# Kernel tuning notes

Measured on AMD Instinct MI355X. Metric: run time of the kernel, lower is better.

## Reference

```python
import jax, jax.numpy as jnp
import numpy as np

L, N, D, B_, T = 4, 4, 2048, 2, 2048  # num_blocks, expansion_rate, dim, batch, seq


def setup_inputs() -> dict:
    key = jax.random.key(0)
    ks = jax.random.split(key, 12)
    f = lambda k, sh, s=0.02: s * jax.random.normal(k, sh, jnp.float32)
    x = jax.random.normal(ks[0], (B_, T, D), jnp.float32)
    # structural torch inits + small noise so grads/kernels are exercised
    eyecols = jnp.stack([jnp.eye(N, dtype=jnp.float32)[:, [i % N]] for i in range(L)])  # [L,N,1]
    A_m = eyecols + f(ks[1], (L, N, 1), 0.05)
    A_r = jnp.broadcast_to(jnp.eye(N, dtype=jnp.float32), (L, N, N)) + f(ks[2], (L, N, N), 0.05)
    Bp = jnp.ones((L, 1, N), jnp.float32) + f(ks[3], (L, 1, N), 0.05)
    W_m = f(ks[4], (L, D, 1))
    W_r = f(ks[5], (L, D, N))
    W_b = f(ks[6], (L, D, N))
    s_a = 0.01 * jnp.ones((L, 1, 1), jnp.float32)
    s_b = 0.01 * jnp.ones((L, 1, 1), jnp.float32)
    dyn_gamma = jnp.ones((L, D), jnp.float32) + f(ks[7], (L, D), 0.05)   # LayerNorm(bias=False)
    norm_gamma = jnp.ones((L, D), jnp.float32) + f(ks[8], (L, D), 0.05)  # per-block norm weight
    norm_beta = f(ks[9], (L, D))                                          # per-block norm bias
    Wblk = f(ks[10], (L, D, D), 1.0) / np.sqrt(D)                         # block = Linear(D, D)
    bblk = f(ks[11], (L, D))
    return dict(x=x, A_m=A_m, A_r=A_r, Bp=Bp, W_m=W_m, W_r=W_r, W_b=W_b,
                s_a=s_a, s_b=s_b, dyn_gamma=dyn_gamma, norm_gamma=norm_gamma,
                norm_beta=norm_beta, Wblk=Wblk, bblk=bblk)


def _ln(x, gamma, beta=None, eps=1e-5):
    mu = jnp.mean(x, axis=-1, keepdims=True)
    var = jnp.mean(jnp.square(x - mu), axis=-1, keepdims=True)
    y = (x - mu) * jax.lax.rsqrt(var + eps) * gamma
    return y if beta is None else y + beta


def reference(x, A_m, A_r, Bp, W_m, W_r, W_b, s_a, s_b,
              dyn_gamma, norm_gamma, norm_beta, Wblk, bblk):
    # hyper branch (n > 0), dynamic=True, pre_norm=True
    H = jnp.repeat(x[:, :, None, :], N, axis=2)  # [B,T,N,D]
    for i in range(L):
        # ---- width connections ----
        Hn = _ln(H, dyn_gamma[i])                                              # dynamic LN, no bias
        Am = A_m[i] + s_a[i] * jnp.tanh(jnp.einsum('btnd,do->btno', Hn, W_m[i]))  # [B,T,N,1]
        Ar = A_r[i] + s_a[i] * jnp.tanh(jnp.einsum('btnd,dm->btnm', Hn, W_r[i]))  # [B,T,N,N]
        WC = jnp.concatenate([Am, Ar], axis=-1)                                # [B,T,N,1+N]
        Ht = jnp.einsum('btnd,btnm->btdm', H, WC)                              # H^T @ WC
        h = Ht[..., 0]                                                         # [B,T,D]
        H = jnp.swapaxes(Ht[..., 1:], -2, -1)                                  # [B,T,N,D]
        # ---- pre-norm + block ----
        h = _ln(h, norm_gamma[i], norm_beta[i])
        h = jnp.einsum('btd,de->bte', h, Wblk[i]) + bblk[i]
        # ---- depth connections ----
        hn = _ln(h, dyn_gamma[i])
        Bv = Bp[i][0] + s_b[i] * jnp.tanh(jnp.einsum('btd,dn->btn', hn, W_b[i]))  # [B,T,N]
        H = H + h[:, :, None, :] * Bv[..., None]
    return H.sum(axis=2)  # [B,T,D]
```

## Files before the change

kernel.cpp:

```cpp
#include <hip/hip_runtime.h>
#include <hip/hip_bf16.h>


#define DD 2048
#define NN 4
#define LL 4
#define NTOK 4096
#define EPSF 1e-5f

typedef __attribute__((ext_vector_type(8))) short bf16x8;
typedef __attribute__((ext_vector_type(4))) float f32x4;

__device__ __forceinline__ float bf2f(short u) {
  union { unsigned int i; float f; } v;
  v.i = ((unsigned int)(unsigned short)u) << 16;
  return v.f;
}
__device__ __forceinline__ short f2bf(float f) {
  union { float f; unsigned int i; } v; v.f = f;
  unsigned int x = v.i;
  return (short)((x + 0x7fffu + ((x >> 16) & 1u)) >> 16);
}
__device__ __forceinline__ float wred(float v) {
#pragma unroll
  for (int off = 32; off > 0; off >>= 1) v += __shfl_xor(v, off, 64);
  return v;
}
__device__ __forceinline__ void ld16(const void* g, void* l) {
  __builtin_amdgcn_global_load_lds(
      (const __attribute__((address_space(1))) void*)g,
      (__attribute__((address_space(3))) void*)l, 16, 0, 0);
}

__global__ __launch_bounds__(256) void prep_pack(
    const float* __restrict__ W_r, const float* __restrict__ W_b,
    short* __restrict__ wrb, short* __restrict__ wbb) {
  const int i = blockIdx.x * 256 + threadIdx.x;
  f32x4 r = *(const f32x4*)(W_r + (size_t)i * 4);
  f32x4 b = *(const f32x4*)(W_b + (size_t)i * 4);
  short ro[4], bo[4];
#pragma unroll
  for (int k = 0; k < 4; k++) { ro[k] = f2bf(r[k]); bo[k] = f2bf(b[k]); }
  *(unsigned long long*)(wrb + (size_t)i * 4) = *(unsigned long long*)ro;
  *(unsigned long long*)(wbb + (size_t)i * 4) = *(unsigned long long*)bo;
}

__global__ __launch_bounds__(64) void prep_sums(
    const float* __restrict__ W_m, const float* __restrict__ W_r,
    const float* __restrict__ W_b, const float* __restrict__ dyn_gamma,
    float* __restrict__ S0w, float* __restrict__ T0d) {
  const int l = blockIdx.x;
  const int lane = threadIdx.x;
  float s[5] = {0, 0, 0, 0, 0}, t[4] = {0, 0, 0, 0};
  for (int d = lane; d < DD; d += 64) {
    const float g = dyn_gamma[l * DD + d];
    s[0] += g * W_m[l * DD + d];
    f32x4 r = *(const f32x4*)(W_r + ((size_t)l * DD + d) * 4);
    f32x4 b = *(const f32x4*)(W_b + ((size_t)l * DD + d) * 4);
#pragma unroll
    for (int m = 0; m < 4; m++) { s[1 + m] += g * r[m]; t[m] += g * b[m]; }
  }
#pragma unroll
  for (int m = 0; m < 5; m++) s[m] = wred(s[m]);
#pragma unroll
  for (int n = 0; n < 4; n++) t[n] = wred(t[n]);
  if (lane == 0) {
#pragma unroll
    for (int m = 0; m < 5; m++) S0w[l * 5 + m] = s[m];
#pragma unroll
    for (int n = 0; n < 4; n++) T0d[l * 4 + n] = t[n];
  }
}

__global__ __launch_bounds__(256) void transpose_wblk(
    const float* __restrict__ W, short* __restrict__ Wt) {
  __shared__ float tile[64][65];
  const int blk = blockIdx.z;
  const int c0 = blockIdx.x * 64;
  const int r0 = blockIdx.y * 64;
  const float* Ws = W + (size_t)blk * DD * DD;
  short* Wd = Wt + (size_t)blk * DD * DD;
  const int tx = threadIdx.x & 63, ty = threadIdx.x >> 6;
#pragma unroll
  for (int r = 0; r < 16; r++) {
    const int row = ty + r * 4;
    tile[row][tx] = Ws[(size_t)(r0 + row) * DD + c0 + tx];
  }
  __syncthreads();
#pragma unroll
  for (int r = 0; r < 16; r++) {
    const int row = ty + r * 4;
    Wd[(size_t)(c0 + row) * DD + r0 + tx] = f2bf(tile[tx][row]);
  }
}

__global__ __launch_bounds__(256) void width0_kernel(
    const float* __restrict__ x, short* __restrict__ Hst,
    short* __restrict__ hnorm, const float* __restrict__ A_m,
    const float* __restrict__ A_r, const float* __restrict__ W_m,
    const short* __restrict__ wrb, const float* __restrict__ s_a,
    const float* __restrict__ dyn_gamma, const float* __restrict__ norm_gamma,
    const float* __restrict__ norm_beta, const float* __restrict__ S0w) {
  const int wave = threadIdx.x >> 6;
  const int lane = threadIdx.x & 63;
  const int tok = blockIdx.x * 4 + wave;
  const int blk = 0;
  const float* dg = dyn_gamma + blk * DD;
  const float* wm = W_m + blk * DD;
  const short* wr = wrb + (size_t)blk * DD * 4;

  bf16x8 hreg[4];
  const float* xr = x + (size_t)tok * DD;
#pragma unroll
  for (int j = 0; j < 4; j++) {
    const int d0 = lane * 8 + j * 512;
    f32x4 a = *(const f32x4*)(xr + d0);
    f32x4 b = *(const f32x4*)(xr + d0 + 4);
    bf16x8 p;
#pragma unroll
    for (int q = 0; q < 4; q++) { p[q] = f2bf(a[q]); p[4 + q] = f2bf(b[q]); }
    hreg[j] = p;
  }

  float sH = 0, sH2 = 0, S1[5] = {0, 0, 0, 0, 0};
#pragma unroll
  for (int j = 0; j < 4; j++) {
    const int d0 = lane * 8 + j * 512;
    f32x4 g0 = *(const f32x4*)(dg + d0), g1 = *(const f32x4*)(dg + d0 + 4);
    f32x4 m0 = *(const f32x4*)(wm + d0), m1 = *(const f32x4*)(wm + d0 + 4);
    bf16x8 wv[4];
#pragma unroll
    for (int p = 0; p < 4; p++)
      wv[p] = *(const bf16x8*)(wr + (size_t)(d0 + 2 * p) * 4);
#pragma unroll
    for (int q = 0; q < 8; q++) {
      const float g = (q < 4) ? g0[q] : g1[q - 4];
      const float wmv = (q < 4) ? m0[q] : m1[q - 4];
      const float hv = bf2f(hreg[j][q]);
      sH += hv; sH2 += hv * hv;
      const float hg = hv * g;
      S1[0] += hg * wmv;
#pragma unroll
      for (int m = 0; m < 4; m++)
        S1[1 + m] += hg * bf2f(wv[q >> 1][(q & 1) * 4 + m]);
    }
  }
  sH = wred(sH); sH2 = wred(sH2);
#pragma unroll
  for (int m = 0; m < 5; m++) S1[m] = wred(S1[m]);

  const float sa = s_a[blk];
  const float mu0 = sH * (1.f / DD);
  const float inv0 = rsqrtf(sH2 * (1.f / DD) - mu0 * mu0 + EPSF);
  float amSum = 0.f, arCol[NN] = {0, 0, 0, 0};
  {
    const float t0 = tanhf(inv0 * (S1[0] - mu0 * S0w[blk * 5 + 0]));
    float tm[NN];
#pragma unroll
    for (int m = 0; m < NN; m++)
      tm[m] = tanhf(inv0 * (S1[1 + m] - mu0 * S0w[blk * 5 + 1 + m]));
#pragma unroll
    for (int n = 0; n < NN; n++) {
      amSum += A_m[blk * NN + n] + sa * t0;
#pragma unroll
      for (int m = 0; m < NN; m++)
        arCol[m] += A_r[blk * NN * NN + n * NN + m] + sa * tm[m];
    }
  }

  short* Ho = Hst + (size_t)tok * NN * DD;
  float hbuf[4][8];
  float sh = 0.f, sh2 = 0.f;
#pragma unroll
  for (int j = 0; j < 4; j++) {
    const int d0 = lane * 8 + j * 512;
    bf16x8 outp[NN];
#pragma unroll
    for (int q = 0; q < 8; q++) {
      const float hv = bf2f(hreg[j][q]);
      const float a0 = hv * amSum;
      hbuf[j][q] = a0; sh += a0; sh2 += a0 * a0;
#pragma unroll
      for (int m = 0; m < NN; m++) outp[m][q] = f2bf(hv * arCol[m]);
    }
#pragma unroll
    for (int m = 0; m < NN; m++) *(bf16x8*)(Ho + m * DD + d0) = outp[m];
  }
  sh = wred(sh); sh2 = wred(sh2);
  const float mu = sh * (1.f / DD);
  const float inv = rsqrtf(sh2 * (1.f / DD) - mu * mu + EPSF);
  const float* ng = norm_gamma + blk * DD;
  const float* nb = norm_beta + blk * DD;
  short* hn = hnorm + (size_t)tok * DD;
#pragma unroll
  for (int j = 0; j < 4; j++) {
    const int d0 = lane * 8 + j * 512;
    f32x4 g0 = *(const f32x4*)(ng + d0), g1 = *(const f32x4*)(ng + d0 + 4);
    f32x4 b0 = *(const f32x4*)(nb + d0), b1 = *(const f32x4*)(nb + d0 + 4);
    bf16x8 o;
#pragma unroll
    for (int q = 0; q < 8; q++) {
      const float g = (q < 4) ? g0[q] : g1[q - 4];
      const float b = (q < 4) ? b0[q] : b1[q - 4];
      o[q] = f2bf((hbuf[j][q] - mu) * inv * g + b);
    }
    *(bf16x8*)(hn + d0) = o;
  }
}

__global__ __launch_bounds__(256) void gemm_kernel(
    const short* __restrict__ A, const short* __restrict__ Bt,
    const float* __restrict__ bias, short* __restrict__ C) {
  __shared__ short lA[2][128 * 64];
  __shared__ short lB[2][128 * 64];
  const int tid = threadIdx.x;
  const int lane = tid & 63;
  const int wave = tid >> 6;
  const int m0 = blockIdx.x * 128, n0 = blockIdx.y * 128;
  const int wm = wave >> 1, wn = wave & 1;

  f32x4 acc[4][4] = {};

#define STAGE(buf, kt)                                                        \
  {                                                                           \
    const int k0 = (kt) * 64;                                                 \
    _Pragma("unroll") for (int c = 0; c < 4; c++) {                           \
      const int idx = c * 256 + tid;                                          \
      const int row = idx >> 3;                                               \
      const int colsw = (((idx & 7) ^ (row & 7)) * 8);                        \
      ld16(A + (size_t)(m0 + row) * DD + k0 + colsw,                          \
           (char*)&lA[buf][0] + idx * 16);                                    \
      ld16(Bt + (size_t)(n0 + row) * DD + k0 + colsw,                         \
           (char*)&lB[buf][0] + idx * 16);                                    \
    }                                                                         \
  }

  STAGE(0, 0);
  __syncthreads();

  for (int kt = 0; kt < 32; ++kt) {
    const int cur = kt & 1;
    if (kt < 31) STAGE(cur ^ 1, kt + 1);
    const char* bufA = (const char*)&lA[cur][0];
    const char* bufB = (const char*)&lB[cur][0];
#pragma unroll
    for (int kk = 0; kk < 2; ++kk) {
      const int gsw = (kk * 64 + (lane >> 4) * 16) ^ ((lane & 7) << 4);
      bf16x8 af[4], bfr[4];
#pragma unroll
      for (int m = 0; m < 4; m++) {
        const int r = wm * 64 + m * 16 + (lane & 15);
        af[m] = *(const bf16x8*)(bufA + r * 128 + gsw);
      }
#pragma unroll
      for (int n = 0; n < 4; n++) {
        const int r = wn * 64 + n * 16 + (lane & 15);
        bfr[n] = *(const bf16x8*)(bufB + r * 128 + gsw);
      }
#pragma unroll
      for (int m = 0; m < 4; m++)
#pragma unroll
        for (int n = 0; n < 4; n++)
          acc[m][n] = __builtin_amdgcn_mfma_f32_16x16x32_bf16(
              af[m], bfr[n], acc[m][n], 0, 0, 0);
    }
    __syncthreads();
  }
#undef STAGE

#pragma unroll
  for (int n = 0; n < 4; n++) {
    const int col = n0 + wn * 64 + n * 16 + (lane & 15);
    const float bv = bias[col];
#pragma unroll
    for (int m = 0; m < 4; m++) {
      const int rbase = m0 + wm * 64 + m * 16 + ((lane >> 4) << 2);
#pragma unroll
      for (int j = 0; j < 4; j++)
        C[(size_t)(rbase + j) * DD + col] = f2bf(acc[m][n][j] + bv);
    }
  }
}

__global__ __launch_bounds__(256) void fused_dw(
    const short* __restrict__ h2, short* __restrict__ Hst,
    short* __restrict__ hnorm, const float* __restrict__ Bp,
    const short* __restrict__ wbb, const float* __restrict__ s_b,
    const float* __restrict__ A_m, const float* __restrict__ A_r,
    const float* __restrict__ W_m, const short* __restrict__ wrb,
    const float* __restrict__ s_a, const float* __restrict__ dyn_gamma,
    const float* __restrict__ norm_gamma, const float* __restrict__ norm_beta,
    const float* __restrict__ S0w, const float* __restrict__ T0d, int blk) {
  const int wave = threadIdx.x >> 6;
  const int lane = threadIdx.x & 63;
  const int tok = blockIdx.x * 4 + wave;
  const int nblk = blk + 1;
  const short* hr = h2 + (size_t)tok * DD;
  short* Ho = Hst + (size_t)tok * NN * DD;

  bf16x8 h2r[4], hold[NN][4];
#pragma unroll
  for (int j = 0; j < 4; j++) {
    const int d0 = lane * 8 + j * 512;
    h2r[j] = *(const bf16x8*)(hr + d0);
#pragma unroll
    for (int n = 0; n < NN; n++)
      hold[n][j] = *(const bf16x8*)(Ho + n * DD + d0);
  }

  const float* dgd = dyn_gamma + blk * DD;
  const short* wb = wbb + (size_t)blk * DD * 4;
  float s1 = 0.f, s2 = 0.f, T1[NN] = {0, 0, 0, 0};
#pragma unroll
  for (int j = 0; j < 4; j++) {
    const int d0 = lane * 8 + j * 512;
    f32x4 g0 = *(const f32x4*)(dgd + d0), g1 = *(const f32x4*)(dgd + d0 + 4);
    bf16x8 wv[4];
#pragma unroll
    for (int p = 0; p < 4; p++)
      wv[p] = *(const bf16x8*)(wb + (size_t)(d0 + 2 * p) * 4);
#pragma unroll
    for (int q = 0; q < 8; q++) {
      const float g = (q < 4) ? g0[q] : g1[q - 4];
      const float hv = bf2f(h2r[j][q]);
      s1 += hv; s2 += hv * hv;
      const float hg = hv * g;
#pragma unroll
      for (int n = 0; n < NN; n++)
        T1[n] += hg * bf2f(wv[q >> 1][(q & 1) * 4 + n]);
    }
  }
  s1 = wred(s1); s2 = wred(s2);
#pragma unroll
  for (int n = 0; n < NN; n++) T1[n] = wred(T1[n]);
  float Bv[NN];
  {
    const float mu = s1 * (1.f / DD);
    const float inv = rsqrtf(s2 * (1.f / DD) - mu * mu + EPSF);
    const float sb = s_b[blk];
#pragma unroll
    for (int n = 0; n < NN; n++)
      Bv[n] = Bp[blk * NN + n] +
              sb * tanhf(inv * (T1[n] - mu * T0d[blk * NN + n]));
  }
#pragma unroll
  for (int n = 0; n < NN; n++)
#pragma unroll
    for (int j = 0; j < 4; j++) {
      bf16x8 o;
#pragma unroll
      for (int q = 0; q < 8; q++)
        o[q] = f2bf(bf2f(hold[n][j][q]) + bf2f(h2r[j][q]) * Bv[n]);
      hold[n][j] = o;
    }

  const float* dg = dyn_gamma + nblk * DD;
  const float* wm = W_m + nblk * DD;
  const short* wr = wrb + (size_t)nblk * DD * 4;
  float sH[NN] = {0, 0, 0, 0}, sH2[NN] = {0, 0, 0, 0};
  float S1[NN][5];
#pragma unroll
  for (int n = 0; n < NN; n++)
#pragma unroll
    for (int m = 0; m < 5; m++) S1[n][m] = 0.f;

#pragma unroll
  for (int j = 0; j < 4; j++) {
    const int d0 = lane * 8 + j * 512;
    f32x4 g0 = *(const f32x4*)(dg + d0), g1 = *(const f32x4*)(dg + d0 + 4);
    f32x4 m0 = *(const f32x4*)(wm + d0), m1 = *(const f32x4*)(wm + d0 + 4);
    bf16x8 wv[4];
#pragma unroll
    for (int p = 0; p < 4; p++)
      wv[p] = *(const bf16x8*)(wr + (size_t)(d0 + 2 * p) * 4);
#pragma unroll
    for (int q = 0; q < 8; q++) {
      const float g = (q < 4) ? g0[q] : g1[q - 4];
      const float wmv = (q < 4) ? m0[q] : m1[q - 4];
      float gw[5];
      gw[0] = g * wmv;
#pragma unroll
      for (int m = 0; m < 4; m++)
        gw[1 + m] = g * bf2f(wv[q >> 1][(q & 1) * 4 + m]);
#pragma unroll
      for (int n = 0; n < NN; n++) {
        const float hv = bf2f(hold[n][j][q]);
        sH[n] += hv; sH2[n] += hv * hv;
#pragma unroll
        for (int m = 0; m < 5; m++) S1[n][m] += hv * gw[m];
      }
    }
  }
#pragma unroll
  for (int n = 0; n < NN; n++) { sH[n] = wred(sH[n]); sH2[n] = wred(sH2[n]); }
#pragma unroll
  for (int n = 0; n < NN; n++)
#pragma unroll
    for (int m = 0; m < 5; m++) S1[n][m] = wred(S1[n][m]);

  const float sa = s_a[nblk];
  float Am[NN], Ar[NN][NN];
#pragma unroll
  for (int n = 0; n < NN; n++) {
    const float mu = sH[n] * (1.f / DD);
    const float var = sH2[n] * (1.f / DD) - mu * mu;
    const float inv = rsqrtf(var + EPSF);
    Am[n] = A_m[nblk * NN + n] +
            sa * tanhf(inv * (S1[n][0] - mu * S0w[nblk * 5 + 0]));
#pragma unroll
    for (int m = 0; m < NN; m++)
      Ar[n][m] = A_r[nblk * NN * NN + n * NN + m] +
                 sa * tanhf(inv * (S1[n][1 + m] - mu * S0w[nblk * 5 + 1 + m]));
  }

  float hbuf[4][8];
  float sh = 0.f, sh2 = 0.f;
#pragma unroll
  for (int j = 0; j < 4; j++) {
    const int d0 = lane * 8 + j * 512;
    bf16x8 outp[NN];
#pragma unroll
    for (int q = 0; q < 8; q++) {
      float a0 = 0.f, am0 = 0.f, am1 = 0.f, am2 = 0.f, am3 = 0.f;
#pragma unroll
      for (int n = 0; n < NN; n++) {
        const float hv = bf2f(hold[n][j][q]);
        a0 += hv * Am[n];
        am0 += hv * Ar[n][0];
        am1 += hv * Ar[n][1];
        am2 += hv * Ar[n][2];
        am3 += hv * Ar[n][3];
      }
      hbuf[j][q] = a0; sh += a0; sh2 += a0 * a0;
      outp[0][q] = f2bf(am0); outp[1][q] = f2bf(am1);
      outp[2][q] = f2bf(am2); outp[3][q] = f2bf(am3);
    }
#pragma unroll
    for (int m = 0; m < NN; m++) *(bf16x8*)(Ho + m * DD + d0) = outp[m];
  }
  sh = wred(sh); sh2 = wred(sh2);
  const float mu = sh * (1.f / DD);
  const float inv = rsqrtf(sh2 * (1.f / DD) - mu * mu + EPSF);
  const float* ng = norm_gamma + nblk * DD;
  const float* nb = norm_beta + nblk * DD;
  short* hn = hnorm + (size_t)tok * DD;
#pragma unroll
  for (int j = 0; j < 4; j++) {
    const int d0 = lane * 8 + j * 512;
    f32x4 g0 = *(const f32x4*)(ng + d0), g1 = *(const f32x4*)(ng + d0 + 4);
    f32x4 b0 = *(const f32x4*)(nb + d0), b1 = *(const f32x4*)(nb + d0 + 4);
    bf16x8 o;
#pragma unroll
    for (int q = 0; q < 8; q++) {
      const float g = (q < 4) ? g0[q] : g1[q - 4];
      const float b = (q < 4) ? b0[q] : b1[q - 4];
      o[q] = f2bf((hbuf[j][q] - mu) * inv * g + b);
    }
    *(bf16x8*)(hn + d0) = o;
  }
}

__global__ __launch_bounds__(256) void depth_last(
    const short* __restrict__ h2, const short* __restrict__ Hst,
    float* __restrict__ out, const float* __restrict__ Bp,
    const short* __restrict__ wbb, const float* __restrict__ s_b,
    const float* __restrict__ dyn_gamma, const float* __restrict__ T0d,
    int blk) {
  const int wave = threadIdx.x >> 6;
  const int lane = threadIdx.x & 63;
  const int tok = blockIdx.x * 4 + wave;
  const short* hr = h2 + (size_t)tok * DD;
  const float* dg = dyn_gamma + blk * DD;
  const short* wb = wbb + (size_t)blk * DD * 4;

  bf16x8 h2r[4];
  float s1 = 0.f, s2 = 0.f, T1[NN] = {0, 0, 0, 0};
#pragma unroll
  for (int j = 0; j < 4; j++) {
    const int d0 = lane * 8 + j * 512;
    h2r[j] = *(const bf16x8*)(hr + d0);
    f32x4 g0 = *(const f32x4*)(dg + d0), g1 = *(const f32x4*)(dg + d0 + 4);
    bf16x8 wv[4];
#pragma unroll
    for (int p = 0; p < 4; p++)
      wv[p] = *(const bf16x8*)(wb + (size_t)(d0 + 2 * p) * 4);
#pragma unroll
    for (int q = 0; q < 8; q++) {
      const float g = (q < 4) ? g0[q] : g1[q - 4];
      const float hv = bf2f(h2r[j][q]);
      s1 += hv; s2 += hv * hv;
      const float hg = hv * g;
#pragma unroll
      for (int n = 0; n < NN; n++)
        T1[n] += hg * bf2f(wv[q >> 1][(q & 1) * 4 + n]);
    }
  }
  s1 = wred(s1); s2 = wred(s2);
#pragma unroll
  for (int n = 0; n < NN; n++) T1[n] = wred(T1[n]);
  const float mu = s1 * (1.f / DD);
  const float inv = rsqrtf(s2 * (1.f / DD) - mu * mu + EPSF);
  const float sb = s_b[blk];
  float bsum = 0.f;
#pragma unroll
  for (int n = 0; n < NN; n++)
    bsum += Bp[blk * NN + n] + sb * tanhf(inv * (T1[n] - mu * T0d[blk * NN + n]));

  const short* Ho = Hst + (size_t)tok * NN * DD;
  float* orow = out + (size_t)tok * DD;
#pragma unroll
  for (int j = 0; j < 4; j++) {
    const int d0 = lane * 8 + j * 512;
    bf16x8 hrow[NN];
#pragma unroll
    for (int n = 0; n < NN; n++) hrow[n] = *(const bf16x8*)(Ho + n * DD + d0);
    f32x4 o0, o1;
#pragma unroll
    for (int q = 0; q < 8; q++) {
      const float hv = bf2f(h2r[j][q]);
      float s = hv * bsum;
#pragma unroll
      for (int n = 0; n < NN; n++) s += bf2f(hrow[n][q]);
      if (q < 4) o0[q] = s; else o1[q - 4] = s;
    }
    *(f32x4*)(orow + d0) = o0;
    *(f32x4*)(orow + d0 + 4) = o1;
  }
}

extern "C" void kernel_launch(void* const* d_in, const int* in_sizes, int n_in,
                              void* d_out, int out_size, void* d_ws,
                              size_t ws_size, hipStream_t stream) {
  const float* x = (const float*)d_in[0];
  const float* A_m = (const float*)d_in[1];
  const float* A_r = (const float*)d_in[2];
  const float* Bp = (const float*)d_in[3];
  const float* W_m = (const float*)d_in[4];
  const float* W_r = (const float*)d_in[5];
  const float* W_b = (const float*)d_in[6];
  const float* s_a = (const float*)d_in[7];
  const float* s_b = (const float*)d_in[8];
  const float* dyn_gamma = (const float*)d_in[9];
  const float* norm_gamma = (const float*)d_in[10];
  const float* norm_beta = (const float*)d_in[11];
  const float* Wblk = (const float*)d_in[12];
  const float* bblk = (const float*)d_in[13];
  float* out = (float*)d_out;

  char* ws = (char*)d_ws;
  short* Hst = (short*)(ws);
  short* hnorm = (short*)(ws + 67108864);
  short* h2 = (short*)(ws + 83886080);
  short* wrb = (short*)(ws + 100663296);
  short* wbb = (short*)(ws + 100663296 + 65536);
  float* S0w = (float*)(ws + 100663296 + 131072);
  float* T0d = (float*)(ws + 100663296 + 131072 + 128);
  short* Wt = (short*)d_out;

  dim3 tb(256);
  prep_pack<<<32, tb, 0, stream>>>(W_r, W_b, wrb, wbb);
  prep_sums<<<4, dim3(64), 0, stream>>>(W_m, W_r, W_b, dyn_gamma, S0w, T0d);
  transpose_wblk<<<dim3(32, 32, 4), tb, 0, stream>>>(Wblk, Wt);
  width0_kernel<<<1024, tb, 0, stream>>>(x, Hst, hnorm, A_m, A_r, W_m, wrb,
                                         s_a, dyn_gamma, norm_gamma, norm_beta,
                                         S0w);
  for (int i = 0; i < LL; i++) {
    gemm_kernel<<<dim3(32, 16), tb, 0, stream>>>(
        hnorm, Wt + (size_t)i * DD * DD, bblk + i * DD, h2);
    if (i < LL - 1)
      fused_dw<<<1024, tb, 0, stream>>>(h2, Hst, hnorm, Bp, wbb, s_b, A_m, A_r,
                                        W_m, wrb, s_a, dyn_gamma, norm_gamma,
                                        norm_beta, S0w, T0d, i);
    else
      depth_last<<<1024, tb, 0, stream>>>(h2, Hst, out, Bp, wbb, s_b,
                                          dyn_gamma, T0d, i);
  }
}
```

Baseline: 392.0 us.

## Fold pre-norm LayerNorm into GEMM epilogue and gamma into packed weights

Stops materialising the normalised block input. The width kernels now write the raw mixed h plus per-token (inv, mu*inv) stats. norm_gamma is folded into the transposed block weight, and precomputed row sums E0/E1 apply the mean-subtraction and beta/bias correction in the GEMM epilogue. dyn_gamma is also prefolded into the packed bf16 W_m/W_r/W_b, which removes gamma loads and multiplies from the width/depth kernels. This cuts a second pass and per-element LN arithmetic, but adds a row_sums kernel, and the mean cancellation now happens after bf16 rounding, which risks precision loss. It also divides norm_beta by norm_gamma.

```diff
diff --git a/kernel.cpp b/kernel.cpp
--- a/kernel.cpp
+++ b/kernel.cpp
@@ -10,6 +10,7 @@
 
 typedef __attribute__((ext_vector_type(8))) short bf16x8;
 typedef __attribute__((ext_vector_type(4))) float f32x4;
+typedef __attribute__((ext_vector_type(2))) float f32x2;
 
 __device__ __forceinline__ float bf2f(short u) {
   union { unsigned int i; float f; } v;
@@ -17,9 +18,10 @@
   return v.f;
 }
 __device__ __forceinline__ short f2bf(float f) {
-  union { float f; unsigned int i; } v; v.f = f;
-  unsigned int x = v.i;
-  return (short)((x + 0x7fffu + ((x >> 16) & 1u)) >> 16);
+  __hip_bfloat16 h = __float2bfloat16(f);
+  short s;
+  __builtin_memcpy(&s, &h, 2);
+  return s;
 }
 __device__ __forceinline__ float wred(float v) {
 #pragma unroll
@@ -33,16 +35,22 @@
 }
 
 __global__ __launch_bounds__(256) void prep_pack(
-    const float* __restrict__ W_r, const float* __restrict__ W_b,
-    short* __restrict__ wrb, short* __restrict__ wbb) {
+    const float* __restrict__ W_m, const float* __restrict__ W_r,
+    const float* __restrict__ W_b, const float* __restrict__ dyn_gamma,
+    const float* __restrict__ norm_gamma, const float* __restrict__ norm_beta,
+    short* __restrict__ gwm, short* __restrict__ gwr, short* __restrict__ gwb,
+    float* __restrict__ rb) {
   const int i = blockIdx.x * 256 + threadIdx.x;
+  const float g = dyn_gamma[i];
+  gwm[i] = f2bf(g * W_m[i]);
   f32x4 r = *(const f32x4*)(W_r + (size_t)i * 4);
   f32x4 b = *(const f32x4*)(W_b + (size_t)i * 4);
   short ro[4], bo[4];
 #pragma unroll
-  for (int k = 0; k < 4; k++) { ro[k] = f2bf(r[k]); bo[k] = f2bf(b[k]); }
-  *(unsigned long long*)(wrb + (size_t)i * 4) = *(unsigned long long*)ro;
-  *(unsigned long long*)(wbb + (size_t)i * 4) = *(unsigned long long*)bo;
+  for (int k = 0; k < 4; k++) { ro[k] = f2bf(g * r[k]); bo[k] = f2bf(g * b[k]); }
+  *(unsigned long long*)(gwr + (size_t)i * 4) = *(unsigned long long*)ro;
+  *(unsigned long long*)(gwb + (size_t)i * 4) = *(unsigned long long*)bo;
+  rb[i] = norm_beta[i] / norm_gamma[i];
 }
 
 __global__ __launch_bounds__(64) void prep_sums(
@@ -73,7 +81,8 @@
 }
 
 __global__ __launch_bounds__(256) void transpose_wblk(
-    const float* __restrict__ W, short* __restrict__ Wt) {
+    const float* __restrict__ W, const float* __restrict__ norm_gamma,
+    short* __restrict__ Wt) {
   __shared__ float tile[64][65];
   const int blk = blockIdx.z;
   const int c0 = blockIdx.x * 64;
@@ -86,28 +95,56 @@
     const int row = ty + r * 4;
     tile[row][tx] = Ws[(size_t)(r0 + row) * DD + c0 + tx];
   }
+  const float gsc = norm_gamma[blk * DD + r0 + tx];
   __syncthreads();
 #pragma unroll
   for (int r = 0; r < 16; r++) {
     const int row = ty + r * 4;
-    Wd[(size_t)(c0 + row) * DD + r0 + tx] = f2bf(tile[tx][row]);
+    Wd[(size_t)(c0 + row) * DD + r0 + tx] = f2bf(tile[tx][row] * gsc);
+  }
+}
+
+__global__ __launch_bounds__(256) void row_sums(
+    const short* __restrict__ Wt, const float* __restrict__ rb,
+    const float* __restrict__ bblk, float* __restrict__ E0,
+    float* __restrict__ E1) {
+  const int l = blockIdx.y;
+  const int e = blockIdx.x * 4 + (threadIdx.x >> 6);
+  const int lane = threadIdx.x & 63;
+  const short* row = Wt + ((size_t)l * DD + e) * DD;
+  const float* rbl = rb + l * DD;
+  float s1 = 0.f, s0 = 0.f;
+#pragma unroll
+  for (int it = 0; it < 4; it++) {
+    const int d0 = lane * 8 + it * 512;
+    bf16x8 w = *(const bf16x8*)(row + d0);
+    f32x4 r0 = *(const f32x4*)(rbl + d0), r1 = *(const f32x4*)(rbl + d0 + 4);
+#pragma unroll
+    for (int q = 0; q < 8; q++) {
+      const float wq = bf2f(w[q]);
+      s1 += wq;
+      s0 += wq * ((q < 4) ? r0[q] : r1[q - 4]);
+    }
+  }
+  s1 = wred(s1); s0 = wred(s0);
+  if (lane == 0) {
+    E1[l * DD + e] = s1;
+    E0[l * DD + e] = s0 + bblk[l * DD + e];
   }
 }
 
 __global__ __launch_bounds__(256) void width0_kernel(
     const float* __restrict__ x, short* __restrict__ Hst,
-    short* __restrict__ hnorm, const float* __restrict__ A_m,
-    const float* __restrict__ A_r, const float* __restrict__ W_m,
-    const short* __restrict__ wrb, const float* __restrict__ s_a,
-    const float* __restrict__ dyn_gamma, const float* __restrict__ norm_gamma,
-    const float* __restrict__ norm_beta, const float* __restrict__ S0w) {
+    short* __restrict__ hout, f32x2* __restrict__ tst,
+    const float* __restrict__ A_m, const float* __restrict__ A_r,
+    const short* __restrict__ gwm, const short* __restrict__ gwr,
+    const float* __restrict__ s_a, const float* __restrict__ S0w) {
   const int wave = threadIdx.x >> 6;
   const int lane = threadIdx.x & 63;
   const int tok = blockIdx.x * 4 + wave;
   const int blk = 0;
-  const float* dg = dyn_gamma + blk * DD;
-  const float* wm = W_m + blk * DD;
-  const short* wr = wrb + (size_t)blk * DD * 4;
+  const short* wm = gwm + blk * DD;
+  const short* wr = gwr + (size_t)blk * DD * 4;
 
   bf16x8 hreg[4];
   const float* xr = x + (size_t)tok * DD;
@@ -126,23 +163,19 @@
 #pragma unroll
   for (int j = 0; j < 4; j++) {
     const int d0 = lane * 8 + j * 512;
-    f32x4 g0 = *(const f32x4*)(dg + d0), g1 = *(const f32x4*)(dg + d0 + 4);
-    f32x4 m0 = *(const f32x4*)(wm + d0), m1 = *(const f32x4*)(wm + d0 + 4);
+    bf16x8 mv = *(const bf16x8*)(wm + d0);
     bf16x8 wv[4];
 #pragma unroll
     for (int p = 0; p < 4; p++)
       wv[p] = *(const bf16x8*)(wr + (size_t)(d0 + 2 * p) * 4);
 #pragma unroll
     for (int q = 0; q < 8; q++) {
-      const float g = (q < 4) ? g0[q] : g1[q - 4];
-      const float wmv = (q < 4) ? m0[q] : m1[q - 4];
       const float hv = bf2f(hreg[j][q]);
       sH += hv; sH2 += hv * hv;
-      const float hg = hv * g;
-      S1[0] += hg * wmv;
+      S1[0] += hv * bf2f(mv[q]);
 #pragma unroll
       for (int m = 0; m < 4; m++)
-        S1[1 + m] += hg * bf2f(wv[q >> 1][(q & 1) * 4 + m]);
+        S1[1 + m] += hv * bf2f(wv[q >> 1][(q & 1) * 4 + m]);
     }
   }
   sH = wred(sH); sH2 = wred(sH2);
@@ -169,48 +202,38 @@
   }
 
   short* Ho = Hst + (size_t)tok * NN * DD;
-  float hbuf[4][8];
+  short* hw = hout + (size_t)tok * DD;
   float sh = 0.f, sh2 = 0.f;
 #pragma unroll
   for (int j = 0; j < 4; j++) {
     const int d0 = lane * 8 + j * 512;
-    bf16x8 outp[NN];
+    bf16x8 outp[NN], ho;
 #pragma unroll
     for (int q = 0; q < 8; q++) {
       const float hv = bf2f(hreg[j][q]);
       const float a0 = hv * amSum;
-      hbuf[j][q] = a0; sh += a0; sh2 += a0 * a0;
+      sh += a0; sh2 += a0 * a0;
+      ho[q] = f2bf(a0);
 #pragma unroll
       for (int m = 0; m < NN; m++) outp[m][q] = f2bf(hv * arCol[m]);
     }
+    *(bf16x8*)(hw + d0) = ho;
 #pragma unroll
     for (int m = 0; m < NN; m++) *(bf16x8*)(Ho + m * DD + d0) = outp[m];
   }
   sh = wred(sh); sh2 = wred(sh2);
-  const float mu = sh * (1.f / DD);
-  const float inv = rsqrtf(sh2 * (1.f / DD) - mu * mu + EPSF);
-  const float* ng = norm_gamma + blk * DD;
-  const float* nb = norm_beta + blk * DD;
-  short* hn = hnorm + (size_t)tok * DD;
-#pragma unroll
-  for (int j = 0; j < 4; j++) {
-    const int d0 = lane * 8 + j * 512;
-    f32x4 g0 = *(const f32x4*)(ng + d0), g1 = *(const f32x4*)(ng + d0 + 4);
-    f32x4 b0 = *(const f32x4*)(nb + d0), b1 = *(const f32x4*)(nb + d0 + 4);
-    bf16x8 o;
-#pragma unroll
-    for (int q = 0; q < 8; q++) {
-      const float g = (q < 4) ? g0[q] : g1[q - 4];
-      const float b = (q < 4) ? b0[q] : b1[q - 4];
-      o[q] = f2bf((hbuf[j][q] - mu) * inv * g + b);
-    }
-    *(bf16x8*)(hn + d0) = o;
+  if (lane == 0) {
+    const float mu = sh * (1.f / DD);
+    const float inv = rsqrtf(sh2 * (1.f / DD) - mu * mu + EPSF);
+    f32x2 t; t[0] = inv; t[1] = mu * inv;
+    tst[tok] = t;
   }
 }
 
 __global__ __launch_bounds__(256) void gemm_kernel(
     const short* __restrict__ A, const short* __restrict__ Bt,
-    const float* __restrict__ bias, short* __restrict__ C) {
+    const f32x2* __restrict__ tst, const float* __restrict__ E0,
+    const float* __restrict__ E1, short* __restrict__ C) {
   __shared__ short lA[2][128 * 64];
   __shared__ short lB[2][128 * 64];
   const int tid = threadIdx.x;
@@ -268,28 +291,36 @@
   }
 #undef STAGE
 
+  float e0c[4], e1c[4];
+  int cols[4];
 #pragma unroll
   for (int n = 0; n < 4; n++) {
-    const int col = n0 + wn * 64 + n * 16 + (lane & 15);
-    const float bv = bias[col];
-#pragma unroll
-    for (int m = 0; m < 4; m++) {
-      const int rbase = m0 + wm * 64 + m * 16 + ((lane >> 4) << 2);
-#pragma unroll
-      for (int j = 0; j < 4; j++)
-        C[(size_t)(rbase + j) * DD + col] = f2bf(acc[m][n][j] + bv);
+    cols[n] = n0 + wn * 64 + n * 16 + (lane & 15);
+    e0c[n] = E0[cols[n]];
+    e1c[n] = E1[cols[n]];
+  }
+#pragma unroll
+  for (int m = 0; m < 4; m++) {
+    const int rbase = m0 + wm * 64 + m * 16 + ((lane >> 4) << 2);
+#pragma unroll
+    for (int j = 0; j < 4; j++) {
+      const int row = rbase + j;
+      const f32x2 iv = tst[row];
+#pragma unroll
+      for (int n = 0; n < 4; n++)
+        C[(size_t)row * DD + cols[n]] =
+            f2bf(iv[0] * acc[m][n][j] - iv[1] * e1c[n] + e0c[n]);
     }
   }
 }
 
 __global__ __launch_bounds__(256) void fused_dw(
     const short* __restrict__ h2, short* __restrict__ Hst,
-    short* __restrict__ hnorm, const float* __restrict__ Bp,
-    const short* __restrict__ wbb, const float* __restrict__ s_b,
-    const float* __restrict__ A_m, const float* __restrict__ A_r,
-    const float* __restrict__ W_m, const short* __restrict__ wrb,
-    const float* __restrict__ s_a, const float* __restrict__ dyn_gamma,
-    const float* __restrict__ norm_gamma, const float* __restrict__ norm_beta,
+    short* __restrict__ hout, f32x2* __restrict__ tst,
+    const float* __restrict__ Bp, const short* __restrict__ gwb,
+    const float* __restrict__ s_b, const float* __restrict__ A_m,
+    const float* __restrict__ A_r, const short* __restrict__ gwm,
+    const short* __restrict__ gwr, const float* __restrict__ s_a,
     const float* __restrict__ S0w, const float* __restrict__ T0d, int blk) {
   const int wave = threadIdx.x >> 6;
   const int lane = threadIdx.x & 63;
@@ -308,26 +339,22 @@
       hold[n][j] = *(const bf16x8*)(Ho + n * DD + d0);
   }
 
-  const float* dgd = dyn_gamma + blk * DD;
-  const short* wb = wbb + (size_t)blk * DD * 4;
+  const short* wb = gwb + (size_t)blk * DD * 4;
   float s1 = 0.f, s2 = 0.f, T1[NN] = {0, 0, 0, 0};
 #pragma unroll
   for (int j = 0; j < 4; j++) {
     const int d0 = lane * 8 + j * 512;
-    f32x4 g0 = *(const f32x4*)(dgd + d0), g1 = *(const f32x4*)(dgd + d0 + 4);
     bf16x8 wv[4];
 #pragma unroll
     for (int p = 0; p < 4; p++)
       wv[p] = *(const bf16x8*)(wb + (size_t)(d0 + 2 * p) * 4);
 #pragma unroll
     for (int q = 0; q < 8; q++) {
-      const float g = (q < 4) ? g0[q] : g1[q - 4];
       const float hv = bf2f(h2r[j][q]);
       s1 += hv; s2 += hv * hv;
-      const float hg = hv * g;
 #pragma unroll
       for (int n = 0; n < NN; n++)
-        T1[n] += hg * bf2f(wv[q >> 1][(q & 1) * 4 + n]);
+        T1[n] += hv * bf2f(wv[q >> 1][(q & 1) * 4 + n]);
     }
   }
   s1 = wred(s1); s2 = wred(s2);
@@ -354,9 +381,8 @@
       hold[n][j] = o;
     }
 
-  const float* dg = dyn_gamma + nblk * DD;
-  const float* wm = W_m + nblk * DD;
-  const short* wr = wrb + (size_t)nblk * DD * 4;
+  const short* wm = gwm + nblk * DD;
+  const short* wr = gwr + (size_t)nblk * DD * 4;
   float sH[NN] = {0, 0, 0, 0}, sH2[NN] = {0, 0, 0, 0};
   float S1[NN][5];
 #pragma unroll
@@ -367,21 +393,18 @@
 #pragma unroll
   for (int j = 0; j < 4; j++) {
     const int d0 = lane * 8 + j * 512;
-    f32x4 g0 = *(const f32x4*)(dg + d0), g1 = *(const f32x4*)(dg + d0 + 4);
-    f32x4 m0 = *(const f32x4*)(wm + d0), m1 = *(const f32x4*)(wm + d0 + 4);
+    bf16x8 mv = *(const bf16x8*)(wm + d0);
     bf16x8 wv[4];
 #pragma unroll
     for (int p = 0; p < 4; p++)
       wv[p] = *(const bf16x8*)(wr + (size_t)(d0 + 2 * p) * 4);
 #pragma unroll
     for (int q = 0; q < 8; q++) {
-      const float g = (q < 4) ? g0[q] : g1[q - 4];
-      const float wmv = (q < 4) ? m0[q] : m1[q - 4];
       float gw[5];
-      gw[0] = g * wmv;
+      gw[0] = bf2f(mv[q]);
 #pragma unroll
       for (int m = 0; m < 4; m++)
-        gw[1 + m] = g * bf2f(wv[q >> 1][(q & 1) * 4 + m]);
+        gw[1 + m] = bf2f(wv[q >> 1][(q & 1) * 4 + m]);
 #pragma unroll
       for (int n = 0; n < NN; n++) {
         const float hv = bf2f(hold[n][j][q]);
@@ -413,12 +436,12 @@
                  sa * tanhf(inv * (S1[n][1 + m] - mu * S0w[nblk * 5 + 1 + m]));
   }
 
-  float hbuf[4][8];
+  short* hw = hout + (size_t)tok * DD;
   float sh = 0.f, sh2 = 0.f;
 #pragma unroll
   for (int j = 0; j < 4; j++) {
     const int d0 = lane * 8 + j * 512;
-    bf16x8 outp[NN];
+    bf16x8 outp[NN], ho;
 #pragma unroll
     for (int q = 0; q < 8; q++) {
       float a0 = 0.f, am0 = 0.f, am1 = 0.f, am2 = 0.f, am3 = 0.f;
@@ -431,47 +454,34 @@
         am2 += hv * Ar[n][2];
         am3 += hv * Ar[n][3];
       }
-      hbuf[j][q] = a0; sh += a0; sh2 += a0 * a0;
+      sh += a0; sh2 += a0 * a0;
+      ho[q] = f2bf(a0);
       outp[0][q] = f2bf(am0); outp[1][q] = f2bf(am1);
       outp[2][q] = f2bf(am2); outp[3][q] = f2bf(am3);
     }
+    *(bf16x8*)(hw + d0) = ho;
 #pragma unroll
     for (int m = 0; m < NN; m++) *(bf16x8*)(Ho + m * DD + d0) = outp[m];
   }
   sh = wred(sh); sh2 = wred(sh2);
-  const float mu = sh * (1.f / DD);
-  const float inv = rsqrtf(sh2 * (1.f / DD) - mu * mu + EPSF);
-  const float* ng = norm_gamma + nblk * DD;
-  const float* nb = norm_beta + nblk * DD;
-  short* hn = hnorm + (size_t)tok * DD;
-#pragma unroll
-  for (int j = 0; j < 4; j++) {
-    const int d0 = lane * 8 + j * 512;
-    f32x4 g0 = *(const f32x4*)(ng + d0), g1 = *(const f32x4*)(ng + d0 + 4);
-    f32x4 b0 = *(const f32x4*)(nb + d0), b1 = *(const f32x4*)(nb + d0 + 4);
-    bf16x8 o;
-#pragma unroll
-    for (int q = 0; q < 8; q++) {
-      const float g = (q < 4) ? g0[q] : g1[q - 4];
-      const float b = (q < 4) ? b0[q] : b1[q - 4];
-      o[q] = f2bf((hbuf[j][q] - mu) * inv * g + b);
-    }
-    *(bf16x8*)(hn + d0) = o;
+  if (lane == 0) {
+    const float mu = sh * (1.f / DD);
+    const float inv = rsqrtf(sh2 * (1.f / DD) - mu * mu + EPSF);
+    f32x2 t; t[0] = inv; t[1] = mu * inv;
+    tst[tok] = t;
   }
 }
 
 __global__ __launch_bounds__(256) void depth_last(
     const short* __restrict__ h2, const short* __restrict__ Hst,
     float* __restrict__ out, const float* __restrict__ Bp,
-    const short* __restrict__ wbb, const float* __restrict__ s_b,
-    const float* __restrict__ dyn_gamma, const float* __restrict__ T0d,
-    int blk) {
+    const short* __restrict__ gwb, const float* __restrict__ s_b,
+    const float* __restrict__ T0d, int blk) {
   const int wave = threadIdx.x >> 6;
   const int lane = threadIdx.x & 63;
   const int tok = blockIdx.x * 4 + wave;
   const short* hr = h2 + (size_t)tok * DD;
-  const float* dg = dyn_gamma + blk * DD;
-  const short* wb = wbb + (size_t)blk * DD * 4;
+  const short* wb = gwb + (size_t)blk * DD * 4;
 
   bf16x8 h2r[4];
   float s1 = 0.f, s2 = 0.f, T1[NN] = {0, 0, 0, 0};
@@ -479,20 +489,17 @@
   for (int j = 0; j < 4; j++) {
     const int d0 = lane * 8 + j * 512;
     h2r[j] = *(const bf16x8*)(hr + d0);
-    f32x4 g0 = *(const f32x4*)(dg + d0), g1 = *(const f32x4*)(dg + d0 + 4);
     bf16x8 wv[4];
 #pragma unroll
     for (int p = 0; p < 4; p++)
       wv[p] = *(const bf16x8*)(wb + (size_t)(d0 + 2 * p) * 4);
 #pragma unroll
     for (int q = 0; q < 8; q++) {
-      const float g = (q < 4) ? g0[q] : g1[q - 4];
       const float hv = bf2f(h2r[j][q]);
       s1 += hv; s2 += hv * hv;
-      const float hg = hv * g;
 #pragma unroll
       for (int n = 0; n < NN; n++)
-        T1[n] += hg * bf2f(wv[q >> 1][(q & 1) * 4 + n]);
+        T1[n] += hv * bf2f(wv[q >> 1][(q & 1) * 4 + n]);
     }
   }
   s1 = wred(s1); s2 = wred(s2);
@@ -549,30 +556,35 @@
 
   char* ws = (char*)d_ws;
   short* Hst = (short*)(ws);
-  short* hnorm = (short*)(ws + 67108864);
+  short* hbuf = (short*)(ws + 67108864);
   short* h2 = (short*)(ws + 83886080);
-  short* wrb = (short*)(ws + 100663296);
-  short* wbb = (short*)(ws + 100663296 + 65536);
-  float* S0w = (float*)(ws + 100663296 + 131072);
-  float* T0d = (float*)(ws + 100663296 + 131072 + 128);
+  char* aux = ws + 100663296;
+  short* gwm = (short*)(aux);
+  short* gwr = (short*)(aux + 16384);
+  short* gwb = (short*)(aux + 16384 + 65536);
+  float* rb = (float*)(aux + 16384 + 131072);
+  float* S0w = (float*)(aux + 16384 + 131072 + 32768);
+  float* T0d = (float*)(aux + 16384 + 131072 + 32768 + 128);
+  f32x2* tst = (f32x2*)(aux + 16384 + 131072 + 32768 + 256);
+  float* E0 = (float*)(aux + 16384 + 131072 + 32768 + 256 + 32768);
+  float* E1 = E0 + LL * DD;
   short* Wt = (short*)d_out;
 
   dim3 tb(256);
-  prep_pack<<<32, tb, 0, stream>>>(W_r, W_b, wrb, wbb);
+  prep_pack<<<32, tb, 0, stream>>>(W_m, W_r, W_b, dyn_gamma, norm_gamma,
+                                   norm_beta, gwm, gwr, gwb, rb);
   prep_sums<<<4, dim3(64), 0, stream>>>(W_m, W_r, W_b, dyn_gamma, S0w, T0d);
-  transpose_wblk<<<dim3(32, 32, 4), tb, 0, stream>>>(Wblk, Wt);
-  width0_kernel<<<1024, tb, 0, stream>>>(x, Hst, hnorm, A_m, A_r, W_m, wrb,
-                                         s_a, dyn_gamma, norm_gamma, norm_beta,
-                                         S0w);
+  transpose_wblk<<<dim3(32, 32, 4), tb, 0, stream>>>(Wblk, norm_gamma, Wt);
+  row_sums<<<dim3(512, 4), tb, 0, stream>>>(Wt, rb, bblk, E0, E1);
+  width0_kernel<<<1024, tb, 0, stream>>>(x, Hst, hbuf, tst, A_m, A_r, gwm,
+                                         gwr, s_a, S0w);
   for (int i = 0; i < LL; i++) {
     gemm_kernel<<<dim3(32, 16), tb, 0, stream>>>(
-        hnorm, Wt + (size_t)i * DD * DD, bblk + i * DD, h2);
+        hbuf, Wt + (size_t)i * DD * DD, tst, E0 + i * DD, E1 + i * DD, h2);
     if (i < LL - 1)
-      fused_dw<<<1024, tb, 0, stream>>>(h2, Hst, hnorm, Bp, wbb, s_b, A_m, A_r,
-                                        W_m, wrb, s_a, dyn_gamma, norm_gamma,
-                                        norm_beta, S0w, T0d, i);
+      fused_dw<<<1024, tb, 0, stream>>>(h2, Hst, hbuf, tst, Bp, gwb, s_b, A_m,
+                                        A_r, gwm, gwr, s_a, S0w, T0d, i);
     else
-      depth_last<<<1024, tb, 0, stream>>>(h2, Hst, out, Bp, wbb, s_b,
-                                          dyn_gamma, T0d, i);
-  }
-}
+      depth_last<<<1024, tb, 0, stream>>>(h2, Hst, out, Bp, gwb, s_b, T0d, i);
+  }
+}
```

Measured after the change: 390.8 us. No clear change (-0.3%).
